# Kernel optimization log

Hardware: AMD Instinct MI355X
Metric: run time of the kernel (lower is better)

## Reference

```python
import jax, jax.numpy as jnp
import numpy as np

PATCH = 16
LOSS_WEIGHT = 1.0


def setup_inputs() -> dict:
    key = jax.random.key(0)
    cls_score = jax.random.normal(key, (8, 19, 512, 512), dtype=jnp.float32)
    return {"cls_score": cls_score}


def reference(cls_score):
    # Faithful to NuclearLoss(patch_size=16, use_softmax=True, inverse=False,
    # reduction='mean').
    N, C, H, W = cls_score.shape
    p = PATCH
    ph, pw = H // p, W // p
    logits = jax.nn.softmax(cls_score, axis=1)  # softmax over channel dim
    # patchify: (N,C,H,W) -> (N*L, p*p, C) with L = ph*pw
    x = logits.reshape(N, C, ph, p, pw, p)
    x = jnp.einsum('nchpwq->nhwpqc', x)
    patches = x.reshape(N * ph * pw, p * p, C)  # (B, p^2, C)
    # Original: mats = sqrt(bmm(P^T, P)) elementwise, loss = -sum(trace(mat)).
    # Only the diagonal of P^T P is needed: diag_k = sum_i P[i,k]^2.
    diag = jnp.sum(patches * patches, axis=1)          # (B, C)
    loss = -jnp.sum(jnp.sqrt(diag))
    loss = loss / patches.shape[0]                      # reduction='mean'
    return LOSS_WEIGHT * loss
```

## Files before the change

kernel.cpp:

```cpp
#include <hip/hip_runtime.h>
#include <math.h>


#define NIMG 8
#define CCH  19
#define HH   512
#define WW   512
#define CHST (HH * WW)

__global__ __launch_bounds__(256, 4) void nuclear_loss_kernel(
    const float* __restrict__ in, float* __restrict__ out) {
    __shared__ float psum[4 * CCH];

    const int tid  = threadIdx.x;
    const int b    = blockIdx.x;
    const int n    = b >> 8;
    const int rem  = b & 255;
    const int prow = rem >> 3;
    const int creg = rem & 7;
    const int cg   = tid & 15;
    const int row  = (prow << 4) + (tid >> 4);
    const int col  = (creg << 6) + (cg << 2);

    for (int i = tid; i < 4 * CCH; i += 256) psum[i] = 0.0f;
    __syncthreads();

    const float* bp = in + (size_t)n * (size_t)(CCH * CHST)
                         + (size_t)row * WW + col;

    float4 v[CCH];
#pragma unroll
    for (int c = 0; c < CCH; ++c)
        v[c] = *reinterpret_cast<const float4*>(bp + (size_t)c * CHST);

    float sx = 0.f, sy = 0.f, sz = 0.f, sw = 0.f;
#pragma unroll
    for (int c = 0; c < CCH; ++c) {
        v[c].x = __expf(v[c].x); sx += v[c].x;
        v[c].y = __expf(v[c].y); sy += v[c].y;
        v[c].z = __expf(v[c].z); sz += v[c].z;
        v[c].w = __expf(v[c].w); sw += v[c].w;
    }
    const float ix = __builtin_amdgcn_rcpf(sx);
    const float iy = __builtin_amdgcn_rcpf(sy);
    const float iz = __builtin_amdgcn_rcpf(sz);
    const float iw = __builtin_amdgcn_rcpf(sw);

    const int  lane   = tid & 63;
    const bool lead   = (lane < 16) && ((lane & 3) == 0);
    const int  plocal = cg >> 2;

#pragma unroll
    for (int c = 0; c < CCH; ++c) {
        const float tx = v[c].x * ix;
        const float ty = v[c].y * iy;
        const float tz = v[c].z * iz;
        const float tw = v[c].w * iw;
        float x = tx * tx;
        x = fmaf(ty, ty, x);
        x = fmaf(tz, tz, x);
        x = fmaf(tw, tw, x);
        x += __shfl_xor(x, 16, 64);
        x += __shfl_xor(x, 32, 64);
        x += __shfl_down(x, 2, 4);
        x += __shfl_down(x, 1, 4);
        if (lead) atomicAdd(&psum[plocal * CCH + c], x);
    }
    __syncthreads();

    if (tid < 64) {
        float v2 = (tid < 4 * CCH) ? sqrtf(psum[tid]) : 0.0f;
        if (tid + 64 < 4 * CCH) v2 += sqrtf(psum[tid + 64]);
        v2 += __shfl_down(v2, 32, 64);
        v2 += __shfl_down(v2, 16, 64);
        v2 += __shfl_down(v2, 8, 64);
        v2 += __shfl_down(v2, 4, 64);
        v2 += __shfl_down(v2, 2, 64);
        v2 += __shfl_down(v2, 1, 64);
        if (tid == 0) atomicAdd(out, v2 * (-1.0f / 8192.0f));
    }
}

extern "C" void kernel_launch(void* const* d_in, const int* in_sizes, int n_in,
                              void* d_out, int out_size, void* d_ws, size_t ws_size,
                              hipStream_t stream) {
    const float* in = (const float*)d_in[0];
    float* out = (float*)d_out;
    hipMemsetAsync(out, 0, sizeof(float), stream);
    nuclear_loss_kernel<<<2048, 256, 0, stream>>>(in, out);
}
```

Measured before the change: 219.8 us.

## Process half-row patch strips per block with register accumulation across rows

Each block now covers a 16-row by 256-column strip (16 patches) with 512 threads, and each thread handles two row positions, accumulating per-channel sums in registers before reducing. This removes the cross-row shuffles per channel and cuts the number of global atomics and blocks by a factor of four. In exchange, only 512 blocks are launched, which may under-fill the GPU. Holding 19 float4 values plus 19 partial sums per thread raises register pressure under a 512-thread launch bound.

```diff
diff --git a/kernel.cpp b/kernel.cpp
--- a/kernel.cpp
+++ b/kernel.cpp
@@ -8,77 +8,93 @@
 #define WW   512
 #define CHST (HH * WW)
 
-__global__ __launch_bounds__(256, 4) void nuclear_loss_kernel(
+__global__ __launch_bounds__(512, 4) void nuclear_loss_kernel(
     const float* __restrict__ in, float* __restrict__ out) {
-    __shared__ float psum[4 * CCH];
+    __shared__ float psum[16 * CCH];
+    __shared__ float total;
 
-    const int tid  = threadIdx.x;
-    const int b    = blockIdx.x;
-    const int n    = b >> 8;
-    const int rem  = b & 255;
-    const int prow = rem >> 3;
-    const int creg = rem & 7;
-    const int cg   = tid & 15;
-    const int row  = (prow << 4) + (tid >> 4);
-    const int col  = (creg << 6) + (cg << 2);
+    const int tid   = threadIdx.x;
+    const int b     = blockIdx.x;
+    const int n     = b >> 6;
+    const int rem   = b & 63;
+    const int prow  = rem >> 1;
+    const int chalf = rem & 1;
+    const int lane  = tid & 63;
 
-    for (int i = tid; i < 4 * CCH; i += 256) psum[i] = 0.0f;
+    for (int i = tid; i < 16 * CCH; i += 512) psum[i] = 0.0f;
+    if (tid == 0) total = 0.0f;
     __syncthreads();
 
-    const float* bp = in + (size_t)n * (size_t)(CCH * CHST)
-                         + (size_t)row * WW + col;
+    float part[CCH];
+#pragma unroll
+    for (int c = 0; c < CCH; ++c) part[c] = 0.0f;
 
-    float4 v[CCH];
+    const float* nbase = in + (size_t)n * (size_t)(CCH * CHST)
+                            + (size_t)(prow << 4) * WW + (chalf << 8);
+
 #pragma unroll
-    for (int c = 0; c < CCH; ++c)
-        v[c] = *reinterpret_cast<const float4*>(bp + (size_t)c * CHST);
+    for (int it = 0; it < 2; ++it) {
+        const int g    = tid + (it << 9);
+        const int rloc = g >> 6;
+        const int cloc = (g & 63) << 2;
+        const float* bp = nbase + (size_t)rloc * WW + cloc;
 
-    float sx = 0.f, sy = 0.f, sz = 0.f, sw = 0.f;
+        float4 v[CCH];
+#pragma unroll
+        for (int c = 0; c < CCH; ++c)
+            v[c] = *reinterpret_cast<const float4*>(bp + (size_t)c * CHST);
+
+        float sx = 0.f, sy = 0.f, sz = 0.f, sw = 0.f;
+#pragma unroll
+        for (int c = 0; c < CCH; ++c) {
+            v[c].x = __expf(v[c].x); sx += v[c].x;
+            v[c].y = __expf(v[c].y); sy += v[c].y;
+            v[c].z = __expf(v[c].z); sz += v[c].z;
+            v[c].w = __expf(v[c].w); sw += v[c].w;
+        }
+        const float ix = __builtin_amdgcn_rcpf(sx);
+        const float iy = __builtin_amdgcn_rcpf(sy);
+        const float iz = __builtin_amdgcn_rcpf(sz);
+        const float iw = __builtin_amdgcn_rcpf(sw);
+
+#pragma unroll
+        for (int c = 0; c < CCH; ++c) {
+            const float tx = v[c].x * ix;
+            const float ty = v[c].y * iy;
+            const float tz = v[c].z * iz;
+            const float tw = v[c].w * iw;
+            float x = tx * tx;
+            x = fmaf(ty, ty, x);
+            x = fmaf(tz, tz, x);
+            x = fmaf(tw, tw, x);
+            part[c] += x;
+        }
+    }
+
+    const int p = lane >> 2;
 #pragma unroll
     for (int c = 0; c < CCH; ++c) {
-        v[c].x = __expf(v[c].x); sx += v[c].x;
-        v[c].y = __expf(v[c].y); sy += v[c].y;
-        v[c].z = __expf(v[c].z); sz += v[c].z;
-        v[c].w = __expf(v[c].w); sw += v[c].w;
-    }
-    const float ix = __builtin_amdgcn_rcpf(sx);
-    const float iy = __builtin_amdgcn_rcpf(sy);
-    const float iz = __builtin_amdgcn_rcpf(sz);
-    const float iw = __builtin_amdgcn_rcpf(sw);
-
-    const int  lane   = tid & 63;
-    const bool lead   = (lane < 16) && ((lane & 3) == 0);
-    const int  plocal = cg >> 2;
-
-#pragma unroll
-    for (int c = 0; c < CCH; ++c) {
-        const float tx = v[c].x * ix;
-        const float ty = v[c].y * iy;
-        const float tz = v[c].z * iz;
-        const float tw = v[c].w * iw;
-        float x = tx * tx;
-        x = fmaf(ty, ty, x);
-        x = fmaf(tz, tz, x);
-        x = fmaf(tw, tw, x);
-        x += __shfl_xor(x, 16, 64);
-        x += __shfl_xor(x, 32, 64);
+        float x = part[c];
         x += __shfl_down(x, 2, 4);
         x += __shfl_down(x, 1, 4);
-        if (lead) atomicAdd(&psum[plocal * CCH + c], x);
+        if ((lane & 3) == 0)
+            atomicAdd(&psum[p * CCH + c], x);
     }
     __syncthreads();
 
-    if (tid < 64) {
-        float v2 = (tid < 4 * CCH) ? sqrtf(psum[tid]) : 0.0f;
-        if (tid + 64 < 4 * CCH) v2 += sqrtf(psum[tid + 64]);
+    float v2 = 0.0f;
+    if (tid < 16 * CCH) v2 = sqrtf(psum[tid]);
+    if (tid < 320) {
         v2 += __shfl_down(v2, 32, 64);
         v2 += __shfl_down(v2, 16, 64);
         v2 += __shfl_down(v2, 8, 64);
         v2 += __shfl_down(v2, 4, 64);
         v2 += __shfl_down(v2, 2, 64);
         v2 += __shfl_down(v2, 1, 64);
-        if (tid == 0) atomicAdd(out, v2 * (-1.0f / 8192.0f));
+        if (lane == 0) atomicAdd(&total, v2);
     }
+    __syncthreads();
+    if (tid == 0) atomicAdd(out, total * (-1.0f / 8192.0f));
 }
 
 extern "C" void kernel_launch(void* const* d_in, const int* in_sizes, int n_in,
@@ -87,5 +103,5 @@
     const float* in = (const float*)d_in[0];
     float* out = (float*)d_out;
     hipMemsetAsync(out, 0, sizeof(float), stream);
-    nuclear_loss_kernel<<<2048, 256, 0, stream>>>(in, out);
+    nuclear_loss_kernel<<<512, 512, 0, stream>>>(in, out);
 }
```

New measurement: 253.4 us. +15.3%, slower.

## Remap thread-to-pixel layout so patch reductions stay in-wave via DPP

Applied to the files above, without the earlier changes.

Reassigns threads so each wave covers four rows of four 16-column patches, which lets the per-patch channel sums be reduced with four DPP row operations instead of cross-lane shuffles. Each wave's partial sums are written to shared memory without atomics, then combined across waves before the sqrt and the final global atomic. The intent is to cut shuffle and LDS-atomic overhead in a kernel that is mostly memory-bound. Each thread's float4 loads now cover only 16 contiguous floats per row group (4 lanes), which may reduce how well global loads coalesce.

```diff
diff --git a/kernel.cpp b/kernel.cpp
--- a/kernel.cpp
+++ b/kernel.cpp
@@ -8,9 +8,16 @@
 #define WW   512
 #define CHST (HH * WW)
 
+template <int CTRL>
+__device__ __forceinline__ float dpp_add(float x) {
+    int t = __builtin_amdgcn_update_dpp(0, __float_as_int(x), CTRL, 0xF, 0xF, true);
+    return x + __int_as_float(t);
+}
+
 __global__ __launch_bounds__(256, 4) void nuclear_loss_kernel(
     const float* __restrict__ in, float* __restrict__ out) {
-    __shared__ float psum[4 * CCH];
+    __shared__ float psum[4 * 4 * CCH];
+    __shared__ float total;
 
     const int tid  = threadIdx.x;
     const int b    = blockIdx.x;
@@ -18,13 +25,16 @@
     const int rem  = b & 255;
     const int prow = rem >> 3;
     const int creg = rem & 7;
-    const int cg   = tid & 15;
-    const int row  = (prow << 4) + (tid >> 4);
-    const int col  = (creg << 6) + (cg << 2);
+    const int w    = tid >> 6;
+    const int l    = tid & 63;
+    const int p    = l >> 4;
+    const int r    = (l >> 2) & 3;
+    const int cq   = l & 3;
 
-    for (int i = tid; i < 4 * CCH; i += 256) psum[i] = 0.0f;
-    __syncthreads();
+    if (tid == 0) total = 0.0f;
 
+    const int row = (prow << 4) + (w << 2) + r;
+    const int col = (creg << 6) + (p << 4) + (cq << 2);
     const float* bp = in + (size_t)n * (size_t)(CCH * CHST)
                          + (size_t)row * WW + col;
 
@@ -46,9 +56,7 @@
     const float iz = __builtin_amdgcn_rcpf(sz);
     const float iw = __builtin_amdgcn_rcpf(sw);
 
-    const int  lane   = tid & 63;
-    const bool lead   = (lane < 16) && ((lane & 3) == 0);
-    const int  plocal = cg >> 2;
+    const bool lead = ((l & 15) == 12);
 
 #pragma unroll
     for (int c = 0; c < CCH; ++c) {
@@ -60,25 +68,32 @@
         x = fmaf(ty, ty, x);
         x = fmaf(tz, tz, x);
         x = fmaf(tw, tw, x);
-        x += __shfl_xor(x, 16, 64);
-        x += __shfl_xor(x, 32, 64);
-        x += __shfl_down(x, 2, 4);
-        x += __shfl_down(x, 1, 4);
-        if (lead) atomicAdd(&psum[plocal * CCH + c], x);
+        x = dpp_add<0xB1>(x);
+        x = dpp_add<0x4E>(x);
+        x = dpp_add<0x114>(x);
+        x = dpp_add<0x118>(x);
+        if (lead)
+            psum[(w << 2 | p) * CCH + c] = x;
     }
     __syncthreads();
 
-    if (tid < 64) {
-        float v2 = (tid < 4 * CCH) ? sqrtf(psum[tid]) : 0.0f;
-        if (tid + 64 < 4 * CCH) v2 += sqrtf(psum[tid + 64]);
-        v2 += __shfl_down(v2, 32, 64);
-        v2 += __shfl_down(v2, 16, 64);
-        v2 += __shfl_down(v2, 8, 64);
-        v2 += __shfl_down(v2, 4, 64);
-        v2 += __shfl_down(v2, 2, 64);
-        v2 += __shfl_down(v2, 1, 64);
-        if (tid == 0) atomicAdd(out, v2 * (-1.0f / 8192.0f));
+    if (tid < 128) {
+        float acc = 0.0f;
+        if (tid < 4 * CCH) {
+            const float s4 = psum[tid] + psum[76 + tid]
+                           + psum[152 + tid] + psum[228 + tid];
+            acc = sqrtf(s4);
+        }
+        acc += __shfl_down(acc, 32, 64);
+        acc += __shfl_down(acc, 16, 64);
+        acc += __shfl_down(acc, 8, 64);
+        acc += __shfl_down(acc, 4, 64);
+        acc += __shfl_down(acc, 2, 64);
+        acc += __shfl_down(acc, 1, 64);
+        if (l == 0) atomicAdd(&total, acc);
     }
+    __syncthreads();
+    if (tid == 0) atomicAdd(out, total * (-1.0f / 8192.0f));
 }
 
 extern "C" void kernel_launch(void* const* d_in, const int* in_sizes, int n_in,
```

After: 220.1 us. Within noise of the previous version (+0.2%).
